# Optimization experiments

Measured on AMD Instinct MI355X. Metric: run time of the kernel, lower is better.

Reference implementation:

```python
import jax, jax.numpy as jnp
import numpy as np

HEADS = 8
DH = 64      # dim_head
KS = 3       # kernel_size (padding=1, stride=1, dilation=1 -> same-resolution window)


def _unfold3x3(t):
    # t: [b, c, H, W] -> patches [b, c, 9, H, W], window positions in row-major
    # order, matching torch F.unfold channel ordering (c major, kernel pos minor).
    b, c, H, W = t.shape
    tp = jnp.pad(t, ((0, 0), (0, 0), (1, 1), (1, 1)))
    return jnp.stack([tp[:, :, i:i + H, j:j + W]
                      for i in range(KS) for j in range(KS)], axis=2)


def setup_inputs() -> dict:
    key = jax.random.key(0)
    k0, k1, k2, k3 = jax.random.split(key, 4)
    b, c, H, W = 16, 256, 32, 32
    inner = HEADS * DH  # 512
    x = jax.random.normal(k0, (b, c, H, W), jnp.float32)
    Wq = jax.random.normal(k1, (inner, c), jnp.float32) * 0.02      # to_q 1x1 conv
    Wkv = jax.random.normal(k2, (2 * inner, c), jnp.float32) * 0.02  # to_kv 1x1 conv (k=1)
    Wo = jax.random.normal(k3, (c, inner), jnp.float32) * 0.02       # to_out 1x1 conv
    bo = jnp.zeros((c,), jnp.float32)
    return {"x": x, "Wq": Wq, "Wkv": Wkv, "Wo": Wo, "bo": bo}


def reference(x, Wq, Wkv, Wo, bo):
    b, c, H, W = x.shape
    n = H * W
    w = KS * KS
    scale = DH ** -0.5

    # 1x1 convs as channel matmuls
    q = jnp.einsum('bcxy,oc->boxy', x, Wq)               # [b, h*d, H, W]
    q = q.reshape(b, HEADS, DH, n).transpose(0, 1, 3, 2)  # [b, h, n, d]
    kv = jnp.einsum('bcxy,oc->boxy', x, Wkv)
    k, v = jnp.split(kv, 2, axis=1)                       # each [b, h*d, H, W]

    def to_windows(t):
        p = _unfold3x3(t)                                  # [b, h*d, 9, H, W]
        return p.reshape(b, HEADS, DH, w, n).transpose(0, 1, 4, 3, 2)  # [b,h,n,w,d]

    k = to_windows(k)
    v = to_windows(v)

    # einsum over d directly == original repeat(q over w) + elementwise*sum
    dots = jnp.einsum('bhnd,bhnwd->bhnw', q, k) * scale
    attn = jax.nn.softmax(dots, axis=-1)
    out = jnp.einsum('bhnw,bhnwd->bhnd', attn, v)          # [b, h, n, d]
    out = out.transpose(0, 1, 3, 2).reshape(b, HEADS * DH, H, W)
    out = jnp.einsum('bcxy,oc->boxy', out, Wo) + bo[None, :, None, None]
    return (out, attn)
```

## Files before the change

kernel.cpp:

```cpp
#include <hip/hip_runtime.h>

#define NPIX   1024
#define BATCH  16
#define CIN    256
#define NQKV   1536
#define INNER  512
#define HEADS  8
#define DH     64

typedef __attribute__((ext_vector_type(8))) short short8;
typedef __attribute__((ext_vector_type(4))) float f32x4;

__device__ __forceinline__ ushort f2b(float f) {
    union { float f; unsigned u; } v; v.f = f;
    unsigned r = v.u + 0x7fffu + ((v.u >> 16) & 1u);
    return (ushort)(r >> 16);
}
__device__ __forceinline__ float b2f(ushort u) {
    union { float f; unsigned u; } v; v.u = ((unsigned)u) << 16; return v.f;
}
__device__ __forceinline__ void async16(const void* g, void* l) {
    __builtin_amdgcn_global_load_lds((const __attribute__((address_space(1))) void*)g,
                                     (__attribute__((address_space(3))) void*)l, 16, 0, 0);
}

__global__ __launch_bounds__(256) void prep_x(const float* __restrict__ x,
                                              ushort* __restrict__ xT) {
    __shared__ float tile[32][33];
    const int b  = blockIdx.z;
    const int p0 = blockIdx.x * 32;
    const int c0 = blockIdx.y * 32;
    const int tx = threadIdx.x, ty = threadIdx.y;
#pragma unroll
    for (int i = 0; i < 4; i++) {
        int c = ty + i * 8;
        tile[c][tx] = x[(b * CIN + c0 + c) * NPIX + p0 + tx];
    }
    __syncthreads();
#pragma unroll
    for (int i = 0; i < 4; i++) {
        int p = ty + i * 8;
        xT[(b * NPIX + p0 + p) * CIN + c0 + tx] = f2b(tile[tx][p]);
    }
}

__global__ __launch_bounds__(256) void prep_w(const float* __restrict__ Wq,
        const float* __restrict__ Wkv, const float* __restrict__ Wo,
        ushort* __restrict__ Wqkv_b, ushort* __restrict__ Wob) {
    int i = blockIdx.x * 256 + threadIdx.x;
    if (i < NQKV * CIN)
        Wqkv_b[i] = f2b(i < INNER * CIN ? Wq[i] : Wkv[i - INNER * CIN]);
    int j = i - NQKV * CIN;
    if (j >= 0 && j < CIN * INNER)
        Wob[j] = f2b(Wo[j]);
}

__global__ __launch_bounds__(256) void gemm_qkv(const ushort* __restrict__ xT,
        const ushort* __restrict__ Wb, ushort* __restrict__ qkv) {
    __shared__ ushort Ws[128][32];
    __shared__ ushort Xs[128][32];
    const int m0 = blockIdx.x * 128;
    const int n0 = blockIdx.y * 128;
    const int t    = threadIdx.x;
    const int wave = t >> 6, lane = t & 63;
    const int wo = (wave & 1) * 64, wp = (wave >> 1) * 64;
    const int lrow = lane & 15, loct = lane >> 4;

    const int srow = t >> 2;
    const int skb  = (t & 3) * 8;
    const ushort* gA = Wb + (n0 + srow) * CIN + skb;
    const ushort* gB = xT + (m0 + srow) * CIN + skb;
    ushort* ldsA0 = &Ws[wave * 16][0];
    ushort* ldsA1 = &Ws[64 + wave * 16][0];
    ushort* ldsB0 = &Xs[wave * 16][0];
    ushort* ldsB1 = &Xs[64 + wave * 16][0];

    f32x4 acc[4][4];
#pragma unroll
    for (int i = 0; i < 4; i++)
#pragma unroll
        for (int j = 0; j < 4; j++) acc[i][j] = (f32x4){0.f, 0.f, 0.f, 0.f};

    for (int c0 = 0; c0 < CIN; c0 += 32) {
        async16(gA + c0, ldsA0);
        async16(gA + 64 * CIN + c0, ldsA1);
        async16(gB + c0, ldsB0);
        async16(gB + 64 * CIN + c0, ldsB1);
        __syncthreads();
        short8 a[4], bb[4];
#pragma unroll
        for (int i = 0; i < 4; i++)
            a[i] = *reinterpret_cast<const short8*>(&Ws[wo + i * 16 + lrow][loct * 8]);
#pragma unroll
        for (int j = 0; j < 4; j++)
            bb[j] = *reinterpret_cast<const short8*>(&Xs[wp + j * 16 + lrow][loct * 8]);
#pragma unroll
        for (int i = 0; i < 4; i++)
#pragma unroll
            for (int j = 0; j < 4; j++)
                acc[i][j] = __builtin_amdgcn_mfma_f32_16x16x32_bf16(a[i], bb[j], acc[i][j], 0, 0, 0);
        __syncthreads();
    }
#pragma unroll
    for (int i = 0; i < 4; i++)
#pragma unroll
        for (int j = 0; j < 4; j++) {
            int gm = m0 + wp + j * 16 + lrow;
            int go = n0 + wo + i * 16 + loct * 4;
            ushort4 pk = make_ushort4(f2b(acc[i][j].x), f2b(acc[i][j].y),
                                      f2b(acc[i][j].z), f2b(acc[i][j].w));
            *reinterpret_cast<ushort4*>(&qkv[gm * NQKV + go]) = pk;
        }
}

__global__ __launch_bounds__(256) void attn_kernel(const ushort* __restrict__ qkv,
        ushort* __restrict__ po, float* __restrict__ attn_out) {
    const int m    = blockIdx.x * 4 + (threadIdx.x >> 6);
    const int lane = threadIdx.x & 63;
    const int h = lane >> 3, sub = lane & 7;
    const int b = m >> 10;
    const int p = m & 1023;
    const int py = p >> 5, px = p & 31;
    const int hd8 = h * DH + sub * 8;

    short8 qv = *reinterpret_cast<const short8*>(&qkv[m * NQKV + hd8]);
    float qf[8];
#pragma unroll
    for (int j = 0; j < 8; j++) qf[j] = b2f((ushort)qv[j]);

    float dots[9];
    int   nb[9];
    bool  ok[9];
#pragma unroll
    for (int w = 0; w < 9; w++) {
        int dy = w / 3 - 1, dx = w % 3 - 1;
        int ny = py + dy, nx = px + dx;
        bool in = ((unsigned)ny < 32u) && ((unsigned)nx < 32u);
        ok[w] = in;
        int nm = b * NPIX + ny * 32 + nx;
        nb[w] = nm;
        float d = 0.f;
        if (in) {
            short8 kv8 = *reinterpret_cast<const short8*>(&qkv[nm * NQKV + 512 + hd8]);
#pragma unroll
            for (int j = 0; j < 8; j++) d = fmaf(qf[j], b2f((ushort)kv8[j]), d);
        }
        d += __shfl_xor(d, 1);
        d += __shfl_xor(d, 2);
        d += __shfl_xor(d, 4);
        dots[w] = d * 0.125f;
    }

    float mx = dots[0];
#pragma unroll
    for (int w = 1; w < 9; w++) mx = fmaxf(mx, dots[w]);
    float e[9], s = 0.f;
#pragma unroll
    for (int w = 0; w < 9; w++) { e[w] = __expf(dots[w] - mx); s += e[w]; }
    const float inv = 1.f / s;

    float o[8] = {};
#pragma unroll
    for (int w = 0; w < 9; w++) {
        if (ok[w]) {
            short8 vv = *reinterpret_cast<const short8*>(&qkv[nb[w] * NQKV + 1024 + hd8]);
            float pw = e[w] * inv;
#pragma unroll
            for (int j = 0; j < 8; j++) o[j] = fmaf(pw, b2f((ushort)vv[j]), o[j]);
        }
    }
    short8 r;
#pragma unroll
    for (int j = 0; j < 8; j++) r[j] = (short)f2b(o[j]);
    *reinterpret_cast<short8*>(&po[m * INNER + hd8]) = r;

    float* ab = &attn_out[((b * HEADS + h) * NPIX + p) * 9];
    ab[sub] = e[sub] * inv;
    if (sub == 0) ab[8] = e[8] * inv;
}

__global__ __launch_bounds__(256) void gemm_out(const ushort* __restrict__ po,
        const ushort* __restrict__ Wob, const float* __restrict__ bo,
        float* __restrict__ out) {
    __shared__ ushort As[128][32];
    __shared__ ushort Bs[128][32];
    const int m0 = blockIdx.x * 128;
    const int n0 = blockIdx.y * 128;
    const int t    = threadIdx.x;
    const int wave = t >> 6, lane = t & 63;
    const int wm = (wave >> 1) * 64, wn = (wave & 1) * 64;
    const int lrow = lane & 15, loct = lane >> 4;

    const int srow = t >> 2;
    const int skb  = (t & 3) * 8;
    const ushort* gA = po  + (m0 + srow) * INNER + skb;
    const ushort* gB = Wob + (n0 + srow) * INNER + skb;
    ushort* ldsA0 = &As[wave * 16][0];
    ushort* ldsA1 = &As[64 + wave * 16][0];
    ushort* ldsB0 = &Bs[wave * 16][0];
    ushort* ldsB1 = &Bs[64 + wave * 16][0];

    f32x4 acc[4][4];
#pragma unroll
    for (int i = 0; i < 4; i++)
#pragma unroll
        for (int j = 0; j < 4; j++) acc[i][j] = (f32x4){0.f, 0.f, 0.f, 0.f};

    for (int c0 = 0; c0 < INNER; c0 += 32) {
        async16(gA + c0, ldsA0);
        async16(gA + 64 * INNER + c0, ldsA1);
        async16(gB + c0, ldsB0);
        async16(gB + 64 * INNER + c0, ldsB1);
        __syncthreads();
        short8 a[4], bb[4];
#pragma unroll
        for (int i = 0; i < 4; i++)
            a[i] = *reinterpret_cast<const short8*>(&As[wm + i * 16 + lrow][loct * 8]);
#pragma unroll
        for (int j = 0; j < 4; j++)
            bb[j] = *reinterpret_cast<const short8*>(&Bs[wn + j * 16 + lrow][loct * 8]);
#pragma unroll
        for (int i = 0; i < 4; i++)
#pragma unroll
            for (int j = 0; j < 4; j++)
                acc[i][j] = __builtin_amdgcn_mfma_f32_16x16x32_bf16(a[i], bb[j], acc[i][j], 0, 0, 0);
        __syncthreads();
    }
    const int bb_ = m0 >> 10;
    const int p0  = m0 & 1023;
#pragma unroll
    for (int i = 0; i < 4; i++)
#pragma unroll
        for (int j = 0; j < 4; j++) {
            int o  = n0 + wn + j * 16 + lrow;
            int pp = p0 + wm + i * 16 + loct * 4;
            float bias = bo[o];
            float4 v = make_float4(acc[i][j].x + bias, acc[i][j].y + bias,
                                   acc[i][j].z + bias, acc[i][j].w + bias);
            *reinterpret_cast<float4*>(&out[(bb_ * CIN + o) * NPIX + pp]) = v;
        }
}

extern "C" void kernel_launch(void* const* d_in, const int* in_sizes, int n_in,
                              void* d_out, int out_size, void* d_ws, size_t ws_size,
                              hipStream_t stream) {
    const float* x   = (const float*)d_in[0];
    const float* Wq  = (const float*)d_in[1];
    const float* Wkv = (const float*)d_in[2];
    const float* Wo  = (const float*)d_in[3];
    const float* bo  = (const float*)d_in[4];

    float* out  = (float*)d_out;
    float* attn = out + BATCH * CIN * NPIX;

    ushort* xT     = (ushort*)d_ws;
    ushort* Wqkv_b = xT + 16384 * CIN;
    ushort* Wob    = Wqkv_b + NQKV * CIN;
    ushort* qkv    = Wob + CIN * INNER;
    ushort* po     = qkv + 16384 * NQKV;

    prep_x<<<dim3(32, 8, BATCH), dim3(32, 8), 0, stream>>>(x, xT);
    prep_w<<<2048, 256, 0, stream>>>(Wq, Wkv, Wo, Wqkv_b, Wob);

    gemm_qkv<<<dim3(128, 12), 256, 0, stream>>>(xT, Wqkv_b, qkv);

    attn_kernel<<<16384 / 4, 256, 0, stream>>>(qkv, po, attn);

    gemm_out<<<dim3(128, 2), 256, 0, stream>>>(po, Wob, bo, out);
}
```

Baseline: 139.8 us.

## Double-buffer LDS in both GEMMs and swizzle block order for XCD locality

```diff
diff --git a/kernel.cpp b/kernel.cpp
--- a/kernel.cpp
+++ b/kernel.cpp
@@ -57,10 +57,12 @@
 
 __global__ __launch_bounds__(256) void gemm_qkv(const ushort* __restrict__ xT,
         const ushort* __restrict__ Wb, ushort* __restrict__ qkv) {
-    __shared__ ushort Ws[128][32];
-    __shared__ ushort Xs[128][32];
-    const int m0 = blockIdx.x * 128;
-    const int n0 = blockIdx.y * 128;
+    __shared__ ushort As[2][128][32];
+    __shared__ ushort Bs[2][128][32];
+    const int bid = blockIdx.x;
+    const int swz = (bid & 7) * 192 + (bid >> 3);
+    const int m0  = (swz / 12) * 128;
+    const int n0  = (swz % 12) * 128;
     const int t    = threadIdx.x;
     const int wave = t >> 6, lane = t & 63;
     const int wo = (wave & 1) * 64, wp = (wave >> 1) * 64;
@@ -70,10 +72,6 @@
     const int skb  = (t & 3) * 8;
     const ushort* gA = Wb + (n0 + srow) * CIN + skb;
     const ushort* gB = xT + (m0 + srow) * CIN + skb;
-    ushort* ldsA0 = &Ws[wave * 16][0];
-    ushort* ldsA1 = &Ws[64 + wave * 16][0];
-    ushort* ldsB0 = &Xs[wave * 16][0];
-    ushort* ldsB1 = &Xs[64 + wave * 16][0];
 
     f32x4 acc[4][4];
 #pragma unroll
@@ -81,26 +79,37 @@
 #pragma unroll
         for (int j = 0; j < 4; j++) acc[i][j] = (f32x4){0.f, 0.f, 0.f, 0.f};
 
-    for (int c0 = 0; c0 < CIN; c0 += 32) {
-        async16(gA + c0, ldsA0);
-        async16(gA + 64 * CIN + c0, ldsA1);
-        async16(gB + c0, ldsB0);
-        async16(gB + 64 * CIN + c0, ldsB1);
-        __syncthreads();
+#define STAGE1(buf, c0)                                             \
+    do {                                                            \
+        async16(gA + (c0),            &As[buf][wave * 16][0]);      \
+        async16(gA + 64 * CIN + (c0), &As[buf][64 + wave * 16][0]); \
+        async16(gB + (c0),            &Bs[buf][wave * 16][0]);      \
+        async16(gB + 64 * CIN + (c0), &Bs[buf][64 + wave * 16][0]); \
+    } while (0)
+
+    STAGE1(0, 0);
+    __syncthreads();
+    int cur = 0;
+    const int NT = CIN / 32;
+    for (int it = 0; it < NT; ++it) {
+        if (it + 1 < NT) STAGE1(cur ^ 1, (it + 1) * 32);
         short8 a[4], bb[4];
 #pragma unroll
         for (int i = 0; i < 4; i++)
-            a[i] = *reinterpret_cast<const short8*>(&Ws[wo + i * 16 + lrow][loct * 8]);
+            a[i] = *reinterpret_cast<const short8*>(&As[cur][wo + i * 16 + lrow][loct * 8]);
 #pragma unroll
         for (int j = 0; j < 4; j++)
-            bb[j] = *reinterpret_cast<const short8*>(&Xs[wp + j * 16 + lrow][loct * 8]);
+            bb[j] = *reinterpret_cast<const short8*>(&Bs[cur][wp + j * 16 + lrow][loct * 8]);
 #pragma unroll
         for (int i = 0; i < 4; i++)
 #pragma unroll
             for (int j = 0; j < 4; j++)
                 acc[i][j] = __builtin_amdgcn_mfma_f32_16x16x32_bf16(a[i], bb[j], acc[i][j], 0, 0, 0);
         __syncthreads();
-    }
+        cur ^= 1;
+    }
+#undef STAGE1
+
 #pragma unroll
     for (int i = 0; i < 4; i++)
 #pragma unroll
@@ -115,7 +124,9 @@
 
 __global__ __launch_bounds__(256) void attn_kernel(const ushort* __restrict__ qkv,
         ushort* __restrict__ po, float* __restrict__ attn_out) {
-    const int m    = blockIdx.x * 4 + (threadIdx.x >> 6);
+    const int bid = blockIdx.x;
+    const int swz = (bid & 7) * 512 + (bid >> 3);
+    const int m    = swz * 4 + (threadIdx.x >> 6);
     const int lane = threadIdx.x & 63;
     const int h = lane >> 3, sub = lane & 7;
     const int b = m >> 10;
@@ -182,8 +193,8 @@
 __global__ __launch_bounds__(256) void gemm_out(const ushort* __restrict__ po,
         const ushort* __restrict__ Wob, const float* __restrict__ bo,
         float* __restrict__ out) {
-    __shared__ ushort As[128][32];
-    __shared__ ushort Bs[128][32];
+    __shared__ ushort As[2][128][32];
+    __shared__ ushort Bs[2][128][32];
     const int m0 = blockIdx.x * 128;
     const int n0 = blockIdx.y * 128;
     const int t    = threadIdx.x;
@@ -195,10 +206,6 @@
     const int skb  = (t & 3) * 8;
     const ushort* gA = po  + (m0 + srow) * INNER + skb;
     const ushort* gB = Wob + (n0 + srow) * INNER + skb;
-    ushort* ldsA0 = &As[wave * 16][0];
-    ushort* ldsA1 = &As[64 + wave * 16][0];
-    ushort* ldsB0 = &Bs[wave * 16][0];
-    ushort* ldsB1 = &Bs[64 + wave * 16][0];
 
     f32x4 acc[4][4];
 #pragma unroll
@@ -206,26 +213,37 @@
 #pragma unroll
         for (int j = 0; j < 4; j++) acc[i][j] = (f32x4){0.f, 0.f, 0.f, 0.f};
 
-    for (int c0 = 0; c0 < INNER; c0 += 32) {
-        async16(gA + c0, ldsA0);
-        async16(gA + 64 * INNER + c0, ldsA1);
-        async16(gB + c0, ldsB0);
-        async16(gB + 64 * INNER + c0, ldsB1);
-        __syncthreads();
+#define STAGE2(buf, c0)                                               \
+    do {                                                              \
+        async16(gA + (c0),              &As[buf][wave * 16][0]);      \
+        async16(gA + 64 * INNER + (c0), &As[buf][64 + wave * 16][0]); \
+        async16(gB + (c0),              &Bs[buf][wave * 16][0]);      \
+        async16(gB + 64 * INNER + (c0), &Bs[buf][64 + wave * 16][0]); \
+    } while (0)
+
+    STAGE2(0, 0);
+    __syncthreads();
+    int cur = 0;
+    const int NT = INNER / 32;
+    for (int it = 0; it < NT; ++it) {
+        if (it + 1 < NT) STAGE2(cur ^ 1, (it + 1) * 32);
         short8 a[4], bb[4];
 #pragma unroll
         for (int i = 0; i < 4; i++)
-            a[i] = *reinterpret_cast<const short8*>(&As[wm + i * 16 + lrow][loct * 8]);
+            a[i] = *reinterpret_cast<const short8*>(&As[cur][wm + i * 16 + lrow][loct * 8]);
 #pragma unroll
         for (int j = 0; j < 4; j++)
-            bb[j] = *reinterpret_cast<const short8*>(&Bs[wn + j * 16 + lrow][loct * 8]);
+            bb[j] = *reinterpret_cast<const short8*>(&Bs[cur][wn + j * 16 + lrow][loct * 8]);
 #pragma unroll
         for (int i = 0; i < 4; i++)
 #pragma unroll
             for (int j = 0; j < 4; j++)
                 acc[i][j] = __builtin_amdgcn_mfma_f32_16x16x32_bf16(a[i], bb[j], acc[i][j], 0, 0, 0);
         __syncthreads();
-    }
+        cur ^= 1;
+    }
+#undef STAGE2
+
     const int bb_ = m0 >> 10;
     const int p0  = m0 & 1023;
 #pragma unroll
@@ -262,7 +280,7 @@
     prep_x<<<dim3(32, 8, BATCH), dim3(32, 8), 0, stream>>>(x, xT);
     prep_w<<<2048, 256, 0, stream>>>(Wq, Wkv, Wo, Wqkv_b, Wob);
 
-    gemm_qkv<<<dim3(128, 12), 256, 0, stream>>>(xT, Wqkv_b, qkv);
+    gemm_qkv<<<1536, 256, 0, stream>>>(xT, Wqkv_b, qkv);
 
     attn_kernel<<<16384 / 4, 256, 0, stream>>>(qkv, po, attn);
 
```

New measurement: 139.8 us. About the same (+0.1%).
